# Optimization experiments

Hardware: AMD Instinct MI355X
Metric: run time of the kernel (lower is better)

Reference implementation:

```python
import jax, jax.numpy as jnp
import numpy as np

N_NODES = 50000
N_EDGES = 200000
IN_DIM = 512
HID = 2000
LAT = 128


def setup_inputs() -> dict:
    key = jax.random.key(0)
    ks = jax.random.split(key, 6)
    x = jax.random.normal(ks[0], (N_NODES, IN_DIM), dtype=jnp.float32)
    edge_index = jax.random.randint(ks[1], (2, N_EDGES), 0, N_NODES, dtype=jnp.int64)
    # glorot-ish scales so ReLU/Sigmoid stay in a sane range
    W1 = jax.random.normal(ks[2], (IN_DIM, HID), dtype=jnp.float32) * (1.0 / np.sqrt(IN_DIM))
    b1 = jnp.zeros((HID,), dtype=jnp.float32)
    W2 = jax.random.normal(ks[3], (HID, LAT), dtype=jnp.float32) * (1.0 / np.sqrt(HID))
    b2 = jnp.zeros((LAT,), dtype=jnp.float32)
    return {"x": x, "edge_index": edge_index, "W1": W1, "b1": b1, "W2": W2, "b2": b2}


def gcn_conv(x, edge_index, W, b):
    """PyG GCNConv: D^-1/2 (A+I) D^-1/2 (X W) + b, unit edge weights."""
    n = x.shape[0]
    loops = jnp.arange(n, dtype=edge_index.dtype)
    row = jnp.concatenate([edge_index[0], loops])  # source nodes
    col = jnp.concatenate([edge_index[1], loops])  # target nodes
    deg = jax.ops.segment_sum(jnp.ones_like(col, dtype=x.dtype), col, num_segments=n)
    dis = jnp.where(deg > 0, jax.lax.rsqrt(deg), 0.0)  # deg^-1/2, inf -> 0
    norm = dis[row] * dis[col]                         # [E+N]
    h = x @ W                                          # transform first: [N, out]
    msg = h[row] * norm[:, None]                       # gather + normalize: [E+N, out]
    out = jax.ops.segment_sum(msg, col, num_segments=n)  # scatter-add
    return out + b


def reference(x, edge_index, W1, b1, W2, b2):
    h = jax.nn.relu(gcn_conv(x, edge_index, W1, b1))
    return jax.nn.sigmoid(gcn_conv(h, edge_index, W2, b2))
```

## Files before the change

### kernel.cpp

```cpp
#include <hip/hip_runtime.h>
#include <hip/hip_fp16.h>

#define NN 50000
#define NE 200000
#define IND 512
#define HIDD 2000
#define LATD 128

#define M_PAD 50176
#define N1_PAD 2048
#define MT1 392
#define NBLK 196

typedef _Float16 f16x8 __attribute__((ext_vector_type(8)));
typedef float f32x4 __attribute__((ext_vector_type(4)));

__device__ __forceinline__ void gload_lds16(const _Float16* g, _Float16* l) {
    __builtin_amdgcn_global_load_lds(
        (const __attribute__((address_space(1))) unsigned int*)g,
        (__attribute__((address_space(3))) unsigned int*)l,
        16, 0, 0);
}

__global__ void k_degree(const int* __restrict__ col, int* __restrict__ deg) {
    int e = blockIdx.x * 256 + threadIdx.x;
    if (e < NE) atomicAdd(&deg[col[e]], 1);
}

__global__ void k_dis(const int* __restrict__ deg, float* __restrict__ dis) {
    int i = blockIdx.x * 256 + threadIdx.x;
    if (i < NN) dis[i] = rsqrtf((float)deg[i] + 1.0f);
}

__global__ void k_bsum(const int* __restrict__ deg, int* __restrict__ bsum) {
    __shared__ int sm[4];
    int i = blockIdx.x * 256 + threadIdx.x;
    int v = (i < NN) ? deg[i] : 0;
    #pragma unroll
    for (int off = 32; off; off >>= 1) v += __shfl_down(v, off, 64);
    if ((threadIdx.x & 63) == 0) sm[threadIdx.x >> 6] = v;
    __syncthreads();
    if (threadIdx.x == 0) bsum[blockIdx.x] = sm[0] + sm[1] + sm[2] + sm[3];
}

__global__ void k_bscan(int* __restrict__ bsum) {
    __shared__ int sm[256];
    int tid = threadIdx.x;
    int v = (tid < NBLK) ? bsum[tid] : 0;
    sm[tid] = v;
    __syncthreads();
    #pragma unroll
    for (int off = 1; off < 256; off <<= 1) {
        int t = (tid >= off) ? sm[tid - off] : 0;
        __syncthreads();
        sm[tid] += t;
        __syncthreads();
    }
    if (tid < NBLK) bsum[tid] = sm[tid] - v;
}

__global__ void k_scan_final(const int* __restrict__ deg, const int* __restrict__ bsum,
                             int* __restrict__ row_ptr) {
    __shared__ int sm[256];
    int b = blockIdx.x, tid = threadIdx.x;
    int i = b * 256 + tid;
    int v = (i < NN) ? deg[i] : 0;
    sm[tid] = v;
    __syncthreads();
    #pragma unroll
    for (int off = 1; off < 256; off <<= 1) {
        int t = (tid >= off) ? sm[tid - off] : 0;
        __syncthreads();
        sm[tid] += t;
        __syncthreads();
    }
    if (i < NN) row_ptr[i] = bsum[b] + sm[tid] - v;
    if (i == NN - 1) row_ptr[NN] = bsum[b] + sm[tid];
}

__global__ void k_fill(const int* __restrict__ ei, const int* __restrict__ row_ptr,
                       int* __restrict__ cursor, int* __restrict__ csr_src) {
    int e = blockIdx.x * 256 + threadIdx.x;
    if (e < NE) {
        int r = ei[e], c = ei[NE + e];
        int pos = atomicAdd(&cursor[c], 1);
        csr_src[row_ptr[c] + pos] = r;
    }
}

__global__ void k_transpose_tiled(const float* __restrict__ in,
                                  _Float16* __restrict__ out, int R, int C, int ldo) {
    __shared__ float sm[32][33];
    int c0 = blockIdx.x * 32, r0 = blockIdx.y * 32;
    int tx = threadIdx.x & 31, ty = threadIdx.x >> 5;
    #pragma unroll
    for (int i = 0; i < 4; ++i) {
        int r = r0 + ty + i * 8, c = c0 + tx;
        sm[ty + i * 8][tx] = (r < R && c < C) ? in[(size_t)r * C + c] : 0.f;
    }
    __syncthreads();
    #pragma unroll
    for (int i = 0; i < 4; ++i) {
        int c = c0 + ty + i * 8, r = r0 + tx;
        if (c < C && r < R) out[(size_t)c * ldo + r] = (_Float16)sm[tx][ty + i * 8];
    }
}

__global__ void k_xcvt(const float* __restrict__ in, _Float16* __restrict__ out, int n8) {
    int i = blockIdx.x * 256 + threadIdx.x;
    if (i < n8) {
        float4 a = ((const float4*)in)[i * 2];
        float4 b = ((const float4*)in)[i * 2 + 1];
        f16x8 o;
        o[0] = (_Float16)a.x; o[1] = (_Float16)a.y; o[2] = (_Float16)a.z; o[3] = (_Float16)a.w;
        o[4] = (_Float16)b.x; o[5] = (_Float16)b.y; o[6] = (_Float16)b.z; o[7] = (_Float16)b.w;
        ((f16x8*)out)[i] = o;
    }
}

__global__ void k_gather_x(const _Float16* __restrict__ xh, const int* __restrict__ row_ptr,
                           const int* __restrict__ csr_src, const float* __restrict__ dis,
                           _Float16* __restrict__ Ah) {
    int dst = blockIdx.x * 4 + (threadIdx.x >> 6);
    if (dst >= NN) return;
    int lane = threadIdx.x & 63;
    float dd = dis[dst];
    const f16x8* vb = (const f16x8*)xh;
    f16x8 sv = vb[(size_t)dst * 64 + lane];
    float acc[8];
    #pragma unroll
    for (int q = 0; q < 8; ++q) acc[q] = dd * (float)sv[q];
    int beg = row_ptr[dst], end = row_ptr[dst + 1];
    for (int c = beg; c < end; c += 64) {
        int n = end - c; if (n > 64) n = 64;
        int li = (lane < n) ? csr_src[c + lane] : 0;
        float lns = (lane < n) ? dis[li] : 0.f;
        for (int j = 0; j < n; j += 4) {
            int j1 = j + 1 < n ? j + 1 : n - 1;
            int j2 = j + 2 < n ? j + 2 : n - 1;
            int j3 = j + 3 < n ? j + 3 : n - 1;
            int s0 = __shfl(li, j),  s1 = __shfl(li, j1);
            int s2 = __shfl(li, j2), s3 = __shfl(li, j3);
            float w0 = __shfl(lns, j);
            float w1 = (j + 1 < n) ? __shfl(lns, j1) : 0.f;
            float w2 = (j + 2 < n) ? __shfl(lns, j2) : 0.f;
            float w3 = (j + 3 < n) ? __shfl(lns, j3) : 0.f;
            f16x8 v0 = vb[(size_t)s0 * 64 + lane];
            f16x8 v1 = vb[(size_t)s1 * 64 + lane];
            f16x8 v2 = vb[(size_t)s2 * 64 + lane];
            f16x8 v3 = vb[(size_t)s3 * 64 + lane];
            #pragma unroll
            for (int q = 0; q < 8; ++q)
                acc[q] += w0 * (float)v0[q] + w1 * (float)v1[q]
                        + w2 * (float)v2[q] + w3 * (float)v3[q];
        }
    }
    f16x8 o;
    #pragma unroll
    for (int q = 0; q < 8; ++q) o[q] = (_Float16)(dd * acc[q]);
    *(f16x8*)(Ah + (size_t)dst * IND + lane * 8) = o;
}

__global__ void k_gather_t(const float* __restrict__ t, const int* __restrict__ row_ptr,
                           const int* __restrict__ csr_src, const float* __restrict__ dis,
                           const float* __restrict__ b2, float* __restrict__ out) {
    int dst = blockIdx.x * 4 + (threadIdx.x >> 6);
    if (dst >= NN) return;
    int lane = threadIdx.x & 63;
    float dd = dis[dst];
    const float2* vb = (const float2*)t;
    float2 td = vb[(size_t)dst * 64 + lane];
    float accx = dd * td.x, accy = dd * td.y;
    int beg = row_ptr[dst], end = row_ptr[dst + 1];
    for (int c = beg; c < end; c += 64) {
        int n = end - c; if (n > 64) n = 64;
        int li = (lane < n) ? csr_src[c + lane] : 0;
        float lns = (lane < n) ? dis[li] : 0.f;
        for (int j = 0; j < n; j += 4) {
            int j1 = j + 1 < n ? j + 1 : n - 1;
            int j2 = j + 2 < n ? j + 2 : n - 1;
            int j3 = j + 3 < n ? j + 3 : n - 1;
            int s0 = __shfl(li, j),  s1 = __shfl(li, j1);
            int s2 = __shfl(li, j2), s3 = __shfl(li, j3);
            float w0 = __shfl(lns, j);
            float w1 = (j + 1 < n) ? __shfl(lns, j1) : 0.f;
            float w2 = (j + 2 < n) ? __shfl(lns, j2) : 0.f;
            float w3 = (j + 3 < n) ? __shfl(lns, j3) : 0.f;
            float2 v0 = vb[(size_t)s0 * 64 + lane];
            float2 v1 = vb[(size_t)s1 * 64 + lane];
            float2 v2 = vb[(size_t)s2 * 64 + lane];
            float2 v3 = vb[(size_t)s3 * 64 + lane];
            accx += w0 * v0.x + w1 * v1.x + w2 * v2.x + w3 * v3.x;
            accy += w0 * v0.y + w1 * v1.y + w2 * v2.y + w3 * v3.y;
        }
    }
    float2 bb = *(const float2*)(b2 + lane * 2);
    float vx = dd * accx + bb.x;
    float vy = dd * accy + bb.y;
    float2 o;
    o.x = 1.0f / (1.0f + __expf(-vx));
    o.y = 1.0f / (1.0f + __expf(-vy));
    *(float2*)(out + (size_t)dst * LATD + lane * 2) = o;
}

__global__ __launch_bounds__(256, 2) void k_gemm1(
    const _Float16* __restrict__ A,
    const _Float16* __restrict__ Bt,
    const float* __restrict__ bias,
    _Float16* __restrict__ Ch,
    int mT0, int slab)
{
    const int b = blockIdx.x;
    const int mT = mT0 + (b & 7) * slab + ((b >> 3) >> 4);
    const int nT = (b >> 3) & 15;
    const int mBase = mT * 128;
    const int nBase = nT * 128;

    __shared__ __align__(16) _Float16 As[2 * 128 * 32];
    __shared__ __align__(16) _Float16 Bs[2 * 128 * 32];

    const int tid = threadIdx.x;
    const int lane = tid & 63;
    const int w = tid >> 6;

    const int srow = w * 32 + (lane >> 2);
    const int scol = (lane & 3) * 8;
    const _Float16* Ag0 = A + (size_t)(mBase + srow) * IND + scol;
    const _Float16* Ag1 = Ag0 + (size_t)16 * IND;
    const _Float16* Bg0 = Bt + (size_t)(nBase + srow) * IND + scol;
    const _Float16* Bg1 = Bg0 + (size_t)16 * IND;

    const int wm = (w >> 1) * 64;
    const int wn = (w & 1) * 64;
    const int lm = lane & 15;
    const int quad = lane >> 4;

    f32x4 acc[4][4];
    #pragma unroll
    for (int i = 0; i < 4; ++i)
        #pragma unroll
        for (int j = 0; j < 4; ++j)
            acc[i][j] = (f32x4){0.f, 0.f, 0.f, 0.f};

    for (int k0 = 0; k0 < IND; k0 += 64) {
        #pragma unroll
        for (int s = 0; s < 2; ++s) {
            gload_lds16(Ag0 + k0 + s * 32, As + s * 4096 + w * 1024);
            gload_lds16(Ag1 + k0 + s * 32, As + s * 4096 + w * 1024 + 512);
            gload_lds16(Bg0 + k0 + s * 32, Bs + s * 4096 + w * 1024);
            gload_lds16(Bg1 + k0 + s * 32, Bs + s * 4096 + w * 1024 + 512);
        }
        __syncthreads();

        #pragma unroll
        for (int s = 0; s < 2; ++s) {
            f16x8 af[4], bfr[4];
            #pragma unroll
            for (int mi = 0; mi < 4; ++mi)
                af[mi] = *(const f16x8*)&As[s * 4096 + (wm + mi * 16 + lm) * 32 + quad * 8];
            #pragma unroll
            for (int ni = 0; ni < 4; ++ni)
                bfr[ni] = *(const f16x8*)&Bs[s * 4096 + (wn + ni * 16 + lm) * 32 + quad * 8];
            #pragma unroll
            for (int mi = 0; mi < 4; ++mi)
                #pragma unroll
                for (int ni = 0; ni < 4; ++ni)
                    acc[mi][ni] = __builtin_amdgcn_mfma_f32_16x16x32_f16(
                        af[mi], bfr[ni], acc[mi][ni], 0, 0, 0);
        }
        __syncthreads();
    }

    #pragma unroll
    for (int mi = 0; mi < 4; ++mi) {
        #pragma unroll
        for (int ni = 0; ni < 4; ++ni) {
            int col = nBase + wn + ni * 16 + lm;
            float bval = bias[col];
            #pragma unroll
            for (int r = 0; r < 4; ++r) {
                int rowg = mBase + wm + mi * 16 + quad * 4 + r;
                float v = fmaxf(acc[mi][ni][r] + bval, 0.f);
                Ch[(size_t)rowg * N1_PAD + col] = (_Float16)v;
            }
        }
    }
}

__global__ __launch_bounds__(256, 2) void k_gemm2(
    const _Float16* __restrict__ A,
    const _Float16* __restrict__ Bt,
    float* __restrict__ Cf)
{
    __shared__ __align__(16) _Float16 As[2 * 64 * 32];
    __shared__ __align__(16) _Float16 Bs[2 * 128 * 32];

    const int tid = threadIdx.x;
    const int lane = tid & 63;
    const int w = tid >> 6;
    const int mBase = blockIdx.x * 64;

    const int srA = w * 16 + (lane >> 2);
    const int srB = w * 32 + (lane >> 2);
    const int scol = (lane & 3) * 8;
    const _Float16* Ag  = A + (size_t)(mBase + srA) * N1_PAD + scol;
    const _Float16* Bg0 = Bt + (size_t)srB * N1_PAD + scol;
    const _Float16* Bg1 = Bg0 + (size_t)16 * N1_PAD;

    const int wm = (w & 1) * 32;
    const int wn = (w >> 1) * 64;
    const int lm = lane & 15;
    const int quad = lane >> 4;

    f32x4 acc[2][4];
    #pragma unroll
    for (int i = 0; i < 2; ++i)
        #pragma unroll
        for (int j = 0; j < 4; ++j)
            acc[i][j] = (f32x4){0.f, 0.f, 0.f, 0.f};

    for (int k0 = 0; k0 < N1_PAD; k0 += 64) {
        #pragma unroll
        for (int s = 0; s < 2; ++s) {
            gload_lds16(Ag + k0 + s * 32, As + s * 2048 + w * 512);
            gload_lds16(Bg0 + k0 + s * 32, Bs + s * 4096 + w * 1024);
            gload_lds16(Bg1 + k0 + s * 32, Bs + s * 4096 + w * 1024 + 512);
        }
        __syncthreads();

        #pragma unroll
        for (int s = 0; s < 2; ++s) {
            f16x8 af[2], bfr[4];
            #pragma unroll
            for (int mi = 0; mi < 2; ++mi)
                af[mi] = *(const f16x8*)&As[s * 2048 + (wm + mi * 16 + lm) * 32 + quad * 8];
            #pragma unroll
            for (int ni = 0; ni < 4; ++ni)
                bfr[ni] = *(const f16x8*)&Bs[s * 4096 + (wn + ni * 16 + lm) * 32 + quad * 8];
            #pragma unroll
            for (int mi = 0; mi < 2; ++mi)
                #pragma unroll
                for (int ni = 0; ni < 4; ++ni)
                    acc[mi][ni] = __builtin_amdgcn_mfma_f32_16x16x32_f16(
                        af[mi], bfr[ni], acc[mi][ni], 0, 0, 0);
        }
        __syncthreads();
    }

    #pragma unroll
    for (int mi = 0; mi < 2; ++mi) {
        #pragma unroll
        for (int ni = 0; ni < 4; ++ni) {
            int col = wn + ni * 16 + lm;
            #pragma unroll
            for (int r = 0; r < 4; ++r) {
                int rowg = mBase + wm + mi * 16 + quad * 4 + r;
                Cf[(size_t)rowg * LATD + col] = acc[mi][ni][r];
            }
        }
    }
}

extern "C" void kernel_launch(void* const* d_in, const int* in_sizes, int n_in,
                              void* d_out, int out_size, void* d_ws, size_t ws_size,
                              hipStream_t stream) {
    const float* x  = (const float*)d_in[0];
    const int* ei   = (const int*)d_in[1];
    const float* W1 = (const float*)d_in[2];
    const float* b1 = (const float*)d_in[3];
    const float* W2 = (const float*)d_in[4];
    const float* b2 = (const float*)d_in[5];
    float* out = (float*)d_out;

    char* p = (char*)d_ws;
    auto alloc = [&](size_t bytes) {
        char* q = p; p += (bytes + 255) & ~(size_t)255; return q;
    };
    int* deg        = (int*)alloc((size_t)NN * 4);
    int* bsum       = (int*)alloc((size_t)NBLK * 4);
    int* row_ptr    = (int*)alloc((size_t)(NN + 1) * 4);
    int* cursor     = (int*)alloc((size_t)NN * 4);
    int* csr_src    = (int*)alloc((size_t)NE * 4);
    float* dis      = (float*)alloc((size_t)NN * 4);
    float* b1pad    = (float*)alloc((size_t)N1_PAD * 4);
    _Float16* W1T   = (_Float16*)alloc((size_t)N1_PAD * IND * 2);
    _Float16* W2T   = (_Float16*)alloc((size_t)LATD * N1_PAD * 2);
    _Float16* xh    = (_Float16*)alloc((size_t)NN * IND * 2);
    _Float16* Ah    = (_Float16*)alloc((size_t)M_PAD * IND * 2);
    _Float16* h     = (_Float16*)alloc((size_t)M_PAD * N1_PAD * 2);
    float* t        = (float*)alloc((size_t)M_PAD * LATD * 4);

    hipMemsetAsync(deg,    0, (size_t)NN * 4, stream);
    hipMemsetAsync(cursor, 0, (size_t)NN * 4, stream);
    hipMemsetAsync(b1pad,  0, (size_t)N1_PAD * 4, stream);
    hipMemsetAsync(W1T,    0, (size_t)N1_PAD * IND * 2, stream);
    hipMemsetAsync(W2T,    0, (size_t)LATD * N1_PAD * 2, stream);
    hipMemcpyAsync(b1pad, b1, (size_t)HIDD * 4, hipMemcpyDeviceToDevice, stream);

    k_degree<<<(NE + 255) / 256, 256, 0, stream>>>(ei + NE, deg);
    k_dis<<<(NN + 255) / 256, 256, 0, stream>>>(deg, dis);
    k_bsum<<<NBLK, 256, 0, stream>>>(deg, bsum);
    k_bscan<<<1, 256, 0, stream>>>(bsum);
    k_scan_final<<<NBLK, 256, 0, stream>>>(deg, bsum, row_ptr);
    k_fill<<<(NE + 255) / 256, 256, 0, stream>>>(ei, row_ptr, cursor, csr_src);

    {
        dim3 gt1((HIDD + 31) / 32, (IND + 31) / 32);
        k_transpose_tiled<<<gt1, 256, 0, stream>>>(W1, W1T, IND, HIDD, IND);
        dim3 gt2((LATD + 31) / 32, (HIDD + 31) / 32);
        k_transpose_tiled<<<gt2, 256, 0, stream>>>(W2, W2T, HIDD, LATD, N1_PAD);
        k_xcvt<<<(NN * IND / 8 + 255) / 256, 256, 0, stream>>>(x, xh, NN * IND / 8);
    }

    k_gather_x<<<(NN + 3) / 4, 256, 0, stream>>>(xh, row_ptr, csr_src, dis, Ah);

    k_gemm1<<<8 * 25 * 16, 256, 0, stream>>>(Ah, W1T, b1pad, h, 0, 25);
    k_gemm1<<<8 * 24 * 16, 256, 0, stream>>>(Ah, W1T, b1pad, h, 200, 24);
    k_gemm2<<<M_PAD / 64, 256, 0, stream>>>(h, W2T, t);

    k_gather_t<<<(NN + 3) / 4, 256, 0, stream>>>(t, row_ptr, csr_src, dis, b2, out);
}
```

Before: 503.0 us.

## Double-buffer LDS tiles in both GEMM kernels to overlap loads with MFMA

Splits the K loop of both GEMMs into a stage step and a compute step over two LDS buffers, prefetching the next K tile while MFMAs run on the current one. This removes one barrier per iteration and hides global-to-LDS latency. It doubles the LDS footprint per block, which may limit occupancy, and hardcodes the K-iteration counts.

Result: slower. 525.2 us (+4.4%).

```diff
diff --git a/kernel.cpp b/kernel.cpp
--- a/kernel.cpp
+++ b/kernel.cpp
@@ -216,8 +216,8 @@
     const int mBase = mT * 128;
     const int nBase = nT * 128;
 
-    __shared__ __align__(16) _Float16 As[2 * 128 * 32];
-    __shared__ __align__(16) _Float16 Bs[2 * 128 * 32];
+    __shared__ __align__(16) _Float16 As[2 * 8192];
+    __shared__ __align__(16) _Float16 Bs[2 * 8192];
 
     const int tid = threadIdx.x;
     const int lane = tid & 63;
@@ -242,25 +242,25 @@
         for (int j = 0; j < 4; ++j)
             acc[i][j] = (f32x4){0.f, 0.f, 0.f, 0.f};
 
-    for (int k0 = 0; k0 < IND; k0 += 64) {
+    auto STAGE = [&](int buf, int k0) {
         #pragma unroll
         for (int s = 0; s < 2; ++s) {
-            gload_lds16(Ag0 + k0 + s * 32, As + s * 4096 + w * 1024);
-            gload_lds16(Ag1 + k0 + s * 32, As + s * 4096 + w * 1024 + 512);
-            gload_lds16(Bg0 + k0 + s * 32, Bs + s * 4096 + w * 1024);
-            gload_lds16(Bg1 + k0 + s * 32, Bs + s * 4096 + w * 1024 + 512);
-        }
-        __syncthreads();
-
+            gload_lds16(Ag0 + k0 + s * 32, As + buf * 8192 + s * 4096 + w * 1024);
+            gload_lds16(Ag1 + k0 + s * 32, As + buf * 8192 + s * 4096 + w * 1024 + 512);
+            gload_lds16(Bg0 + k0 + s * 32, Bs + buf * 8192 + s * 4096 + w * 1024);
+            gload_lds16(Bg1 + k0 + s * 32, Bs + buf * 8192 + s * 4096 + w * 1024 + 512);
+        }
+    };
+    auto COMPUTE = [&](int buf) {
         #pragma unroll
         for (int s = 0; s < 2; ++s) {
             f16x8 af[4], bfr[4];
             #pragma unroll
             for (int mi = 0; mi < 4; ++mi)
-                af[mi] = *(const f16x8*)&As[s * 4096 + (wm + mi * 16 + lm) * 32 + quad * 8];
+                af[mi] = *(const f16x8*)&As[buf * 8192 + s * 4096 + (wm + mi * 16 + lm) * 32 + quad * 8];
             #pragma unroll
             for (int ni = 0; ni < 4; ++ni)
-                bfr[ni] = *(const f16x8*)&Bs[s * 4096 + (wn + ni * 16 + lm) * 32 + quad * 8];
+                bfr[ni] = *(const f16x8*)&Bs[buf * 8192 + s * 4096 + (wn + ni * 16 + lm) * 32 + quad * 8];
             #pragma unroll
             for (int mi = 0; mi < 4; ++mi)
                 #pragma unroll
@@ -268,8 +268,23 @@
                     acc[mi][ni] = __builtin_amdgcn_mfma_f32_16x16x32_f16(
                         af[mi], bfr[ni], acc[mi][ni], 0, 0, 0);
         }
-        __syncthreads();
-    }
+    };
+
+    STAGE(0, 0);
+    __syncthreads();
+    #pragma unroll 1
+    for (int it = 0; it < 3; ++it) {
+        STAGE(1, (2 * it + 1) * 64);
+        COMPUTE(0);
+        __syncthreads();
+        STAGE(0, (2 * it + 2) * 64);
+        COMPUTE(1);
+        __syncthreads();
+    }
+    STAGE(1, 7 * 64);
+    COMPUTE(0);
+    __syncthreads();
+    COMPUTE(1);
 
     #pragma unroll
     for (int mi = 0; mi < 4; ++mi) {
@@ -292,8 +307,8 @@
     const _Float16* __restrict__ Bt,
     float* __restrict__ Cf)
 {
-    __shared__ __align__(16) _Float16 As[2 * 64 * 32];
-    __shared__ __align__(16) _Float16 Bs[2 * 128 * 32];
+    __shared__ __align__(16) _Float16 As[2 * 4096];
+    __shared__ __align__(16) _Float16 Bs[2 * 8192];
 
     const int tid = threadIdx.x;
     const int lane = tid & 63;
@@ -319,24 +334,24 @@
         for (int j = 0; j < 4; ++j)
             acc[i][j] = (f32x4){0.f, 0.f, 0.f, 0.f};
 
-    for (int k0 = 0; k0 < N1_PAD; k0 += 64) {
+    auto STAGE = [&](int buf, int k0) {
         #pragma unroll
         for (int s = 0; s < 2; ++s) {
-            gload_lds16(Ag + k0 + s * 32, As + s * 2048 + w * 512);
-            gload_lds16(Bg0 + k0 + s * 32, Bs + s * 4096 + w * 1024);
-            gload_lds16(Bg1 + k0 + s * 32, Bs + s * 4096 + w * 1024 + 512);
-        }
-        __syncthreads();
-
+            gload_lds16(Ag + k0 + s * 32, As + buf * 4096 + s * 2048 + w * 512);
+            gload_lds16(Bg0 + k0 + s * 32, Bs + buf * 8192 + s * 4096 + w * 1024);
+            gload_lds16(Bg1 + k0 + s * 32, Bs + buf * 8192 + s * 4096 + w * 1024 + 512);
+        }
+    };
+    auto COMPUTE = [&](int buf) {
         #pragma unroll
         for (int s = 0; s < 2; ++s) {
             f16x8 af[2], bfr[4];
             #pragma unroll
             for (int mi = 0; mi < 2; ++mi)
-                af[mi] = *(const f16x8*)&As[s * 2048 + (wm + mi * 16 + lm) * 32 + quad * 8];
+                af[mi] = *(const f16x8*)&As[buf * 4096 + s * 2048 + (wm + mi * 16 + lm) * 32 + quad * 8];
             #pragma unroll
             for (int ni = 0; ni < 4; ++ni)
-                bfr[ni] = *(const f16x8*)&Bs[s * 4096 + (wn + ni * 16 + lm) * 32 + quad * 8];
+                bfr[ni] = *(const f16x8*)&Bs[buf * 8192 + s * 4096 + (wn + ni * 16 + lm) * 32 + quad * 8];
             #pragma unroll
             for (int mi = 0; mi < 2; ++mi)
                 #pragma unroll
@@ -344,8 +359,23 @@
                     acc[mi][ni] = __builtin_amdgcn_mfma_f32_16x16x32_f16(
                         af[mi], bfr[ni], acc[mi][ni], 0, 0, 0);
         }
-        __syncthreads();
-    }
+    };
+
+    STAGE(0, 0);
+    __syncthreads();
+    #pragma unroll 1
+    for (int it = 0; it < 15; ++it) {
+        STAGE(1, (2 * it + 1) * 64);
+        COMPUTE(0);
+        __syncthreads();
+        STAGE(0, (2 * it + 2) * 64);
+        COMPUTE(1);
+        __syncthreads();
+    }
+    STAGE(1, 31 * 64);
+    COMPUTE(0);
+    __syncthreads();
+    COMPUTE(1);
 
     #pragma unroll
     for (int mi = 0; mi < 2; ++mi) {
```
